# Performance work log

Measured on AMD Instinct MI355X. Metric: run time of the kernel, lower is better.

The kernel has to match this reference:

```python
import jax, jax.numpy as jnp
import numpy as np

N, F_IN, HID, PROJ, K = 10000, 256, 128, 64, 50
E, HEADS = 320000, 8


def _p(key, shape, scale=0.05):
    return jax.random.normal(key, shape, dtype=jnp.float32) * scale


def setup_inputs() -> dict:
    key = jax.random.key(0)
    ks = jax.random.split(key, 20)
    x = jax.random.normal(ks[0], (N, F_IN), dtype=jnp.float32)
    edge_index = jax.random.randint(ks[1], (2, E), 0, N, dtype=jnp.int64)
    return {
        "x": x,
        "edge_index": edge_index,
        "lin1_w": _p(ks[2], (HID, F_IN)), "lin1_b": _p(ks[3], (HID,)),
        "gat1_w": _p(ks[4], (HEADS * HID, F_IN)),
        "gat1_att_src": _p(ks[5], (HEADS, HID)), "gat1_att_dst": _p(ks[6], (HEADS, HID)),
        "gat1_b": _p(ks[7], (HEADS * HID,)),
        "gat2_w": _p(ks[8], (HID, HEADS * HID)),
        "gat2_att_src": _p(ks[9], (1, HID)), "gat2_att_dst": _p(ks[10], (1, HID)),
        "gat2_b": _p(ks[11], (HID,)),
        "proj_w": _p(ks[12], (PROJ, 2 * HID)), "proj_b": _p(ks[13], (PROJ,)),
        "ln_g": jnp.ones((2 * HID,), jnp.float32), "ln_b": jnp.zeros((2 * HID,), jnp.float32),
        "lin_w": _p(ks[14], (64, 4 * HID)), "lin_b": _p(ks[15], (64,)),
    }


def gat_conv(x, src, dst, W, a_src, a_dst, b, concat):
    # PyG GATConv, add_self_loops=False, eval mode (no attention dropout).
    H, C = a_src.shape
    n = x.shape[0]
    h = (x @ W.T).reshape(n, H, C)                      # [N,H,C]
    al_src = jnp.einsum('nhc,hc->nh', h, a_src)          # [N,H]
    al_dst = jnp.einsum('nhc,hc->nh', h, a_dst)
    e = jax.nn.leaky_relu(al_src[src] + al_dst[dst], 0.2)  # [E,H]
    emax = jax.ops.segment_max(e, dst, num_segments=n)
    ex = jnp.exp(e - emax[dst])
    denom = jax.ops.segment_sum(ex, dst, num_segments=n) + 1e-16
    alpha = ex / denom[dst]                              # [E,H]
    out = jax.ops.segment_sum(h[src] * alpha[:, :, None], dst, num_segments=n)  # [N,H,C]
    if concat:
        return out.reshape(n, H * C) + b
    return out.mean(axis=1) + b


def knn_mean(g_score, final, k):
    # dense pairwise sq-distance + top-k (replaces CPU KDTree loop), gather-mean
    sq = jnp.sum(g_score * g_score, axis=1)
    neg_d2 = 2.0 * (g_score @ g_score.T) - sq[:, None] - sq[None, :]
    idx = jax.lax.top_k(jax.lax.stop_gradient(neg_d2), k)[1]  # [N,k]
    return jnp.mean(final[idx], axis=1)                        # [N,2h]


def reference(x, edge_index, lin1_w, lin1_b, gat1_w, gat1_att_src, gat1_att_dst,
              gat1_b, gat2_w, gat2_att_src, gat2_att_dst, gat2_b, proj_w, proj_b,
              ln_g, ln_b, lin_w, lin_b):
    src, dst = edge_index[0], edge_index[1]
    x1 = jax.nn.relu(x @ lin1_w.T + lin1_b)                              # MLP branch
    xg = jax.nn.relu(gat_conv(x, src, dst, gat1_w, gat1_att_src, gat1_att_dst, gat1_b, True))
    x2 = gat_conv(xg, src, dst, gat2_w, gat2_att_src, gat2_att_dst, gat2_b, False)
    final = jnp.concatenate([x1, x2], axis=1)                            # [N,2h]
    g_score = final @ proj_w.T + proj_b                                  # [N,proj]
    sim = knn_mean(g_score, final, K)                                    # [N,2h]
    mu = sim.mean(axis=-1, keepdims=True)
    var = sim.var(axis=-1, keepdims=True)
    sim = (sim - mu) * jax.lax.rsqrt(var + 1e-5) * ln_g + ln_b           # LayerNorm
    out = jnp.concatenate([final, sim], axis=1) @ lin_w.T + lin_b        # [N,64]
    return out
```

## Files before the change

kernel.cpp:

```cpp
#include <hip/hip_runtime.h>

#define FIN 256
#define KNN 50
#define JB  2000
#define CAP 128

static __device__ __forceinline__ float lrelu02(float v){ return v > 0.f ? v : 0.2f*v; }
static __device__ __forceinline__ unsigned fkey(float v){
  unsigned u = __float_as_uint(v);
  return (u & 0x80000000u) ? ~u : (u | 0x80000000u);
}

__global__ __launch_bounds__(256) void k_zero_int(int* p, int n){
  int i = blockIdx.x*256 + threadIdx.x; if (i<n) p[i]=0;
}
__global__ __launch_bounds__(256) void k_count_deg(const int* __restrict__ dstv, int* deg, int E){
  int i = blockIdx.x*256 + threadIdx.x; if (i<E) atomicAdd(&deg[dstv[i]], 1);
}
__global__ __launch_bounds__(256) void k_scan(const int* __restrict__ deg, int* offs, int* cursor, int n){
  __shared__ int buf[256]; __shared__ int carry;
  int t = threadIdx.x;
  if (t==0) carry = 0;
  __syncthreads();
  for (int base=0; base<n; base+=256){
    int v = (base+t<n)? deg[base+t] : 0;
    buf[t]=v; __syncthreads();
    for (int off=1; off<256; off<<=1){
      int add = (t>=off)? buf[t-off] : 0;
      __syncthreads();
      buf[t]+=add; __syncthreads();
    }
    int excl = buf[t]-v+carry;
    if (base+t<n){ offs[base+t]=excl; cursor[base+t]=excl; }
    __syncthreads();
    if (t==0) carry += buf[255];
    __syncthreads();
  }
}
__global__ __launch_bounds__(256) void k_fill_csr(const int* __restrict__ dstv, int* cursor, int* csr, int E){
  int i = blockIdx.x*256 + threadIdx.x;
  if (i<E){ int p=atomicAdd(&cursor[dstv[i]],1); csr[p]=i; }
}
__global__ __launch_bounds__(64) void k_sort_csr_wave(int* csr, const int* __restrict__ offs, const int* __restrict__ deg, int n){
  int node = blockIdx.x; if (node>=n) return;
  int t = threadIdx.x;
  int st = offs[node], d = deg[node];
  __shared__ int buf[256];
  if (d > 256){
    if (t==0){
      for (int a=1;a<d;++a){ int v=csr[st+a]; int b=a-1;
        while (b>=0 && csr[st+b]>v){ csr[st+b+1]=csr[st+b]; --b; }
        csr[st+b+1]=v; }
    }
    return;
  }
  for (int q=t;q<d;q+=64) buf[q]=csr[st+q];
  __syncthreads();
  for (int it=0; it<d; ++it){
    int ph = it & 1;
    for (int pidx=t; 2*pidx+ph+1 < d; pidx+=64){
      int a = 2*pidx+ph;
      int va=buf[a], vb=buf[a+1];
      if (va > vb){ buf[a]=vb; buf[a+1]=va; }
    }
    __syncthreads();
  }
  for (int q=t;q<d;q+=64) csr[st+q]=buf[q];
}

__global__ __launch_bounds__(256) void k_fold(
  const float* __restrict__ W, const float* __restrict__ as8, const float* __restrict__ ad8,
  float* __restrict__ Wf)
{
  int o = blockIdx.x;
  int t = threadIdx.x;
  int h = o & 7;
  const float* av = (o<8) ? (as8 + h*128) : (ad8 + h*128);
  const float* wp = W + (size_t)h*128*256 + t;
  float acc = 0.f;
  #pragma unroll 4
  for (int c=0;c<128;++c) acc += av[c] * wp[(size_t)c*256];
  Wf[o*256+t] = acc;
}

__global__ __launch_bounds__(256) void gemm_bt(
    const float* __restrict__ A, int lda,
    const float* __restrict__ W, int ldw,
    const float* __restrict__ bias,
    float* __restrict__ C, int ldc, int coff,
    int M, int Kdim, int O, int relu,
    int az, int wz, int cz, int bz)
{
  A += (size_t)blockIdx.z * az;
  W += (size_t)blockIdx.z * wz;
  if (bias) bias += (size_t)blockIdx.z * bz;
  coff += blockIdx.z * cz;
  __shared__ float As[32][68];
  __shared__ float Ws[32][68];
  int t  = threadIdx.x;
  int n0 = blockIdx.y * 64;
  int o0 = blockIdx.x * 64;
  int tx = t & 15, ty = t >> 4;
  float acc[4][4] = {};
  int kgrp = t & 7;
  int row  = t >> 3;
  for (int k0 = 0; k0 < Kdim; k0 += 32) {
    #pragma unroll
    for (int p = 0; p < 2; ++p) {
      int r = row + 32*p;
      int n = n0 + r;
      float4 v = make_float4(0.f,0.f,0.f,0.f);
      if (n < M) v = *(const float4*)(A + (size_t)n*lda + k0 + 4*kgrp);
      As[4*kgrp+0][r] = v.x; As[4*kgrp+1][r] = v.y;
      As[4*kgrp+2][r] = v.z; As[4*kgrp+3][r] = v.w;
      int o = o0 + r;
      float4 w = make_float4(0.f,0.f,0.f,0.f);
      if (o < O) w = *(const float4*)(W + (size_t)o*ldw + k0 + 4*kgrp);
      Ws[4*kgrp+0][r] = w.x; Ws[4*kgrp+1][r] = w.y;
      Ws[4*kgrp+2][r] = w.z; Ws[4*kgrp+3][r] = w.w;
    }
    __syncthreads();
    #pragma unroll 8
    for (int kk = 0; kk < 32; ++kk) {
      float4 a = *(const float4*)&As[kk][ty*4];
      float4 w = *(const float4*)&Ws[kk][tx*4];
      float av[4] = {a.x,a.y,a.z,a.w};
      float wv[4] = {w.x,w.y,w.z,w.w};
      #pragma unroll
      for (int i=0;i<4;++i)
        #pragma unroll
        for (int j=0;j<4;++j) acc[i][j] += av[i]*wv[j];
    }
    __syncthreads();
  }
  #pragma unroll
  for (int i=0;i<4;++i) {
    int n = n0 + ty*4 + i;
    if (n >= M) continue;
    #pragma unroll
    for (int j=0;j<4;++j) {
      int o = o0 + tx*4 + j;
      if (o >= O) continue;
      float v = acc[i][j] + (bias ? bias[o] : 0.f);
      if (relu) v = fmaxf(v, 0.f);
      C[(size_t)n*ldc + coff + o] = v;
    }
  }
}

__global__ __launch_bounds__(256) void gemm128(
    const float* __restrict__ A, int lda,
    const float* __restrict__ W, int ldw,
    const float* __restrict__ bias,
    float* __restrict__ C, int ldc, int coff,
    int M, int Kdim, int relu,
    int az, int wz, int cz, int bz)
{
  A += (size_t)blockIdx.z * az;
  W += (size_t)blockIdx.z * wz;
  const float* bp = bias + (size_t)blockIdx.z * bz;
  int ccol = coff + blockIdx.z * cz;
  __shared__ float As[32][132];
  __shared__ float Ws[32][132];
  int t = threadIdx.x;
  int n0 = blockIdx.y * 128;
  int kg = t & 7, rb = t >> 3;
  int tx = t & 15, ty = t >> 4;
  float acc[2][2][4][4] = {};
  for (int k0 = 0; k0 < Kdim; k0 += 32) {
    __syncthreads();
    #pragma unroll
    for (int p = 0; p < 4; ++p) {
      int r = rb + 32*p;
      int n = n0 + r;
      float4 v = make_float4(0.f,0.f,0.f,0.f);
      if (n < M) v = *(const float4*)(A + (size_t)n*lda + k0 + 4*kg);
      As[4*kg+0][r]=v.x; As[4*kg+1][r]=v.y; As[4*kg+2][r]=v.z; As[4*kg+3][r]=v.w;
      float4 w = *(const float4*)(W + (size_t)r*ldw + k0 + 4*kg);
      Ws[4*kg+0][r]=w.x; Ws[4*kg+1][r]=w.y; Ws[4*kg+2][r]=w.z; Ws[4*kg+3][r]=w.w;
    }
    __syncthreads();
    #pragma unroll 8
    for (int kk = 0; kk < 32; ++kk) {
      float4 A0 = *(const float4*)&As[kk][ty*4];
      float4 A1 = *(const float4*)&As[kk][64+ty*4];
      float4 B0 = *(const float4*)&Ws[kk][tx*4];
      float4 B1 = *(const float4*)&Ws[kk][64+tx*4];
      float av[2][4] = {{A0.x,A0.y,A0.z,A0.w},{A1.x,A1.y,A1.z,A1.w}};
      float bv[2][4] = {{B0.x,B0.y,B0.z,B0.w},{B1.x,B1.y,B1.z,B1.w}};
      #pragma unroll
      for (int pi=0;pi<2;++pi)
        #pragma unroll
        for (int pj=0;pj<2;++pj)
          #pragma unroll
          for (int i=0;i<4;++i)
            #pragma unroll
            for (int j=0;j<4;++j)
              acc[pi][pj][i][j] += av[pi][i]*bv[pj][j];
    }
  }
  #pragma unroll
  for (int pi=0;pi<2;++pi)
    #pragma unroll
    for (int i=0;i<4;++i) {
      int n = n0 + pi*64 + ty*4 + i;
      if (n >= M) continue;
      #pragma unroll
      for (int pj=0;pj<2;++pj)
        #pragma unroll
        for (int j=0;j<4;++j) {
          int o = pj*64 + tx*4 + j;
          float v = acc[pi][pj][i][j] + bp[o];
          if (relu) v = fmaxf(v, 0.f);
          C[(size_t)n*ldc + ccol + o] = v;
        }
    }
}

__global__ __launch_bounds__(256) void att_logits(
    const float* __restrict__ hbuf, const float* __restrict__ asrc,
    const float* __restrict__ adst, float* __restrict__ als, float* __restrict__ ald,
    int H, int M)
{
  int gidx = blockIdx.x*256 + threadIdx.x;
  if (gidx >= M*H) return;
  int n = gidx / H, h = gidx % H;
  const float* hp = hbuf + (size_t)n*H*128 + (size_t)h*128;
  const float* as = asrc + h*128;
  const float* ad = adst + h*128;
  float s1=0.f, s2=0.f;
  for (int c=0;c<128;++c){ float v=hp[c]; s1 += v*as[c]; s2 += v*ad[c]; }
  als[gidx]=s1; ald[gidx]=s2;
}

template<int NH>
__global__ __launch_bounds__(256) void gat1_agg_x(
    const float* __restrict__ x, const float* __restrict__ al1,
    const int* __restrict__ csr, const int* __restrict__ offs, const int* __restrict__ deg,
    const int* __restrict__ srcv,
    float* __restrict__ agg, int h0, int M)
{
  const int n = blockIdx.x, t = threadIdx.x;
  const int d = deg[n], st = offs[n];
  const int lane = t & 63, w = t >> 6;
  __shared__ float sh_ald[NH];
  __shared__ float wpart[4*NH];
  __shared__ float emax_s[NH], den_s[NH];
  __shared__ int   s_lds[128];
  __shared__ float alpha_lds[128*NH];
  if (t < NH) sh_ald[t] = al1[(size_t)n*16 + 8 + h0 + t];
  __syncthreads();
  float lm[NH];
  #pragma unroll
  for (int h=0;h<NH;++h) lm[h] = -__builtin_inff();
  for (int q=t; q<d; q+=256) {
    int s = srcv[csr[st+q]];
    float av[NH];
    float4 a0 = *(const float4*)(al1 + (size_t)s*16 + h0);
    av[0]=a0.x; av[1]=a0.y; av[2]=a0.z; av[3]=a0.w;
    if constexpr (NH==8){
      float4 a1 = *(const float4*)(al1 + (size_t)s*16 + h0 + 4);
      av[4]=a1.x; av[5]=a1.y; av[6]=a1.z; av[7]=a1.w;
    }
    #pragma unroll
    for (int h=0;h<NH;++h) lm[h] = fmaxf(lm[h], lrelu02(av[h] + sh_ald[h]));
  }
  #pragma unroll
  for (int h=0;h<NH;++h){
    float v = lm[h];
    for (int off=32;off>0;off>>=1) v = fmaxf(v, __shfl_down(v, off, 64));
    if (lane==0) wpart[w*NH+h] = v;
  }
  __syncthreads();
  if (t < NH)
    emax_s[t] = fmaxf(fmaxf(wpart[t], wpart[NH+t]), fmaxf(wpart[2*NH+t], wpart[3*NH+t]));
  __syncthreads();
  float ls[NH];
  #pragma unroll
  for (int h=0;h<NH;++h) ls[h]=0.f;
  for (int q=t; q<d; q+=256) {
    int s = srcv[csr[st+q]];
    float av[NH];
    float4 a0 = *(const float4*)(al1 + (size_t)s*16 + h0);
    av[0]=a0.x; av[1]=a0.y; av[2]=a0.z; av[3]=a0.w;
    if constexpr (NH==8){
      float4 a1 = *(const float4*)(al1 + (size_t)s*16 + h0 + 4);
      av[4]=a1.x; av[5]=a1.y; av[6]=a1.z; av[7]=a1.w;
    }
    #pragma unroll
    for (int h=0;h<NH;++h) ls[h] += expf(lrelu02(av[h] + sh_ald[h]) - emax_s[h]);
  }
  #pragma unroll
  for (int h=0;h<NH;++h){
    float v = ls[h];
    for (int off=32;off>0;off>>=1) v += __shfl_down(v, off, 64);
    if (lane==0) wpart[w*NH+h] = v;
  }
  __syncthreads();
  if (t < NH)
    den_s[t] = wpart[t] + wpart[NH+t] + wpart[2*NH+t] + wpart[3*NH+t] + 1e-16f;
  float acc[NH];
  #pragma unroll
  for (int h=0;h<NH;++h) acc[h]=0.f;
  for (int c0=0; c0<d; c0+=128) {
    int cl = min(128, d-c0);
    __syncthreads();
    for (int q=t; q<cl; q+=256) s_lds[q] = srcv[csr[st+c0+q]];
    __syncthreads();
    for (int idx=t; idx<cl*NH; idx+=256) {
      int q = idx / NH, h = idx % NH;
      float als = al1[(size_t)s_lds[q]*16 + h0 + h];
      float v = lrelu02(als + sh_ald[h]);
      alpha_lds[q*NH+h] = expf(v - emax_s[h]) / den_s[h];
    }
    __syncthreads();
    for (int q=0; q<cl; ++q) {
      float xv = x[(size_t)s_lds[q]*FIN + t];
      #pragma unroll
      for (int h=0;h<NH;++h) acc[h] += alpha_lds[q*NH+h] * xv;
    }
  }
  #pragma unroll
  for (int h=0;h<NH;++h) agg[(size_t)n*(NH*256) + h*256 + t] = acc[h];
}

__global__ __launch_bounds__(256) void gat2_agg_wave(
  const float* __restrict__ h2, const float* __restrict__ als, const float* __restrict__ ald,
  const int* __restrict__ csr, const int* __restrict__ offs, const int* __restrict__ deg,
  const int* __restrict__ srcv, const float* __restrict__ bias,
  float* __restrict__ cat, int M)
{
  int wid = blockIdx.x*4 + (threadIdx.x>>6);
  int lane = threadIdx.x & 63;
  if (wid >= M) return;
  int d = deg[wid], st = offs[wid];
  float aldn = ald[wid];
  float lm = -__builtin_inff();
  for (int q=lane;q<d;q+=64){ int s=srcv[csr[st+q]]; lm = fmaxf(lm, lrelu02(als[s]+aldn)); }
  #pragma unroll
  for (int m=1;m<64;m<<=1) lm = fmaxf(lm, __shfl_xor(lm, m, 64));
  float ls = 0.f;
  for (int q=lane;q<d;q+=64){ int s=srcv[csr[st+q]]; ls += expf(lrelu02(als[s]+aldn)-lm); }
  #pragma unroll
  for (int m=1;m<64;m<<=1) ls += __shfl_xor(ls, m, 64);
  float den = ls + 1e-16f;
  float a0=0.f, a1=0.f;
  for (int q=0;q<d;++q){
    int s = srcv[csr[st+q]];
    float alpha = expf(lrelu02(als[s]+aldn)-lm)/den;
    float2 hv = *(const float2*)(h2 + (size_t)s*128 + lane*2);
    a0 += alpha*hv.x; a1 += alpha*hv.y;
  }
  a0 += bias[lane*2]; a1 += bias[lane*2+1];
  *(float2*)(cat + (size_t)wid*512 + 128 + lane*2) = make_float2(a0,a1);
}

__global__ __launch_bounds__(256) void k_sq(const float* __restrict__ g, float* sq, int n){
  int i = blockIdx.x*256+threadIdx.x;
  if (i<n){ const float* p=g+(size_t)i*64; float s=0.f; for(int c=0;c<64;++c) s+=p[c]*p[c]; sq[i]=s; }
}
__global__ __launch_bounds__(256) void k_init_topk(unsigned int* tk, int* ti, int n){
  int i = blockIdx.x*256+threadIdx.x;
  if (i<n){ tk[i]=0u; ti[i]=0x7fffffff; }
}

template<int MODE>
__global__ __launch_bounds__(256) void gram128v4(
    const float* __restrict__ G, const float* __restrict__ sqv,
    const unsigned* __restrict__ kth,
    float* __restrict__ slab, int* __restrict__ cnt,
    unsigned* __restrict__ ck, int* __restrict__ ci,
    int j0, int M)
{
  __shared__ float4 GiS[32*16];
  __shared__ float4 GjS[32*32];
  float* Gif = (float*)GiS;
  float* Gjf = (float*)GjS;
  int t = threadIdx.x;
  int i0  = blockIdx.y * 64;
  int jt0 = blockIdx.x * 128;
  int tx = t & 15, ty = t >> 4;
  int kg = t & 7, rw = t >> 3;
  float acc[2][4][4] = {};
  #pragma unroll
  for (int h=0; h<2; ++h) {
    if (h) __syncthreads();
    #pragma unroll
    for (int rr=0; rr<2; ++rr) {
      int r = rw + 32*rr;
      int slotA = (r>>2) ^ kg;
      int gi = i0 + r;
      float4 v = (gi<M) ? *(const float4*)(G + (size_t)gi*64 + h*32 + 4*kg) : make_float4(0,0,0,0);
      Gif[((4*kg+0)*16 + slotA)*4 + (r&3)] = v.x;
      Gif[((4*kg+1)*16 + slotA)*4 + (r&3)] = v.y;
      Gif[((4*kg+2)*16 + slotA)*4 + (r&3)] = v.z;
      Gif[((4*kg+3)*16 + slotA)*4 + (r&3)] = v.w;
    }
    #pragma unroll
    for (int rr=0; rr<4; ++rr) {
      int r = rw + 32*rr;
      int slotB = (r>>2) ^ kg;
      int gj = j0 + jt0 + r;
      float4 w = (gj<M) ? *(const float4*)(G + (size_t)gj*64 + h*32 + 4*kg) : make_float4(0,0,0,0);
      Gjf[((4*kg+0)*32 + slotB)*4 + (r&3)] = w.x;
      Gjf[((4*kg+1)*32 + slotB)*4 + (r&3)] = w.y;
      Gjf[((4*kg+2)*32 + slotB)*4 + (r&3)] = w.z;
      Gjf[((4*kg+3)*32 + slotB)*4 + (r&3)] = w.w;
    }
    __syncthreads();
    #pragma unroll 8
    for (int k=0; k<32; ++k) {
      int kc3 = (k>>2)&7;
      int sa = ty ^ kc3;
      int sb = tx ^ kc3;
      float4 A0 = GiS[k*16 + sa];
      float4 B0 = GjS[k*32 + sb];
      float4 B1 = GjS[k*32 + 16 + sb];
      float av[4] = {A0.x,A0.y,A0.z,A0.w};
      float bv[2][4] = {{B0.x,B0.y,B0.z,B0.w},{B1.x,B1.y,B1.z,B1.w}};
      #pragma unroll
      for (int pj=0;pj<2;++pj)
        #pragma unroll
        for (int i=0;i<4;++i)
          #pragma unroll
          for (int j=0;j<4;++j)
            acc[pj][i][j] += av[i]*bv[pj][j];
    }
  }
  #pragma unroll
  for (int i=0;i<4;++i){
    int ii = i0 + ty*4 + i;
    if (ii >= M) continue;
    float sqi = sqv[ii];
    #pragma unroll
    for (int pj=0;pj<2;++pj){
      int jl0 = jt0 + pj*64 + tx*4;
      if (jl0 >= JB) continue;
      float4 v4;
      v4.x = 2.f*acc[pj][i][0] - sqi - sqv[j0+jl0+0];
      v4.y = 2.f*acc[pj][i][1] - sqi - sqv[j0+jl0+1];
      v4.z = 2.f*acc[pj][i][2] - sqi - sqv[j0+jl0+2];
      v4.w = 2.f*acc[pj][i][3] - sqi - sqv[j0+jl0+3];
      if (MODE == 0) {
        *(float4*)(slab + (size_t)ii*JB + jl0) = v4;
      } else {
        unsigned kt = kth[ii];
        float vv[4] = {v4.x, v4.y, v4.z, v4.w};
        #pragma unroll
        for (int j=0;j<4;++j){
          unsigned key = fkey(vv[j]);
          if (key > kt){
            int pos = atomicAdd(&cnt[ii], 1);
            if (pos < CAP){ ck[(size_t)ii*CAP+pos] = key; ci[(size_t)ii*CAP+pos] = j0+jl0+j; }
          }
        }
      }
    }
  }
}

__global__ __launch_bounds__(256) void topk_radix(
    const float* __restrict__ slab, int j0, int jcount,
    unsigned* __restrict__ tkk, int* __restrict__ tki, unsigned* __restrict__ kth, int M)
{
  __shared__ unsigned keys[JB + KNN];
  __shared__ int hist[256];
  __shared__ int red2[256];
  __shared__ int oldidx[KNN];
  __shared__ int outidx[KNN];
  __shared__ unsigned outkey[KNN];
  __shared__ int b_star, cnt2;
  int i = blockIdx.x, t = threadIdx.x;
  for (int p=t; p<jcount; p+=256) keys[p] = fkey(slab[(size_t)i*JB + p]);
  for (int p=jcount+t; p<JB; p+=256) keys[p] = 0u;
  if (t < KNN){ keys[JB+t] = tkk[(size_t)i*KNN+t]; oldidx[t] = tki[(size_t)i*KNN+t]; }
  if (t == 0) cnt2 = 0;
  __syncthreads();
  const int total = JB + KNN;
  unsigned prefix = 0, pmask = 0;
  int need = KNN;
  #pragma unroll
  for (int pass=0; pass<4; ++pass) {
    int shift = 24 - 8*pass;
    hist[t] = 0; __syncthreads();
    for (int p=t; p<total; p+=256) {
      unsigned k = keys[p];
      if ((k & pmask) == prefix) atomicAdd(&hist[(k>>shift)&255], 1);
    }
    __syncthreads();
    for (int off=1; off<256; off<<=1) {
      int v = (t+off<256) ? hist[t+off] : 0;
      __syncthreads();
      hist[t] += v;
      __syncthreads();
    }
    if (hist[t] >= need && (t==255 || hist[t+1] < need)) b_star = t;
    __syncthreads();
    int b = b_star;
    need -= (b < 255) ? hist[b+1] : 0;
    prefix |= ((unsigned)b) << shift;
    pmask  |= 0xFFu << shift;
    __syncthreads();
  }
  for (int p=t; p<total; p+=256) {
    unsigned k = keys[p];
    if (k > prefix) {
      int pos = atomicAdd(&cnt2, 1);
      outidx[pos] = (p < JB) ? (j0 + p) : oldidx[p-JB];
      outkey[pos] = k;
    }
  }
  __syncthreads();
  int base = cnt2;
  int last = -1;
  for (int it=0; it<need; ++it) {
    int best = 0x7fffffff;
    for (int p=t; p<total; p+=256) {
      if (keys[p] == prefix) {
        int idx = (p < JB) ? (j0 + p) : oldidx[p-JB];
        if (idx > last && idx < best) best = idx;
      }
    }
    red2[t] = best; __syncthreads();
    for (int s=128;s>0;s>>=1){ if (t<s) red2[t] = min(red2[t], red2[t+s]); __syncthreads(); }
    if (t==0) { outidx[base+it] = red2[0]; outkey[base+it] = prefix; }
    last = red2[0];
    __syncthreads();
  }
  if (t < KNN){ tkk[(size_t)i*KNN+t] = outkey[t]; tki[(size_t)i*KNN+t] = outidx[t]; }
  if (t == 0) kth[i] = prefix;
}

__global__ __launch_bounds__(256) void topk_fast(
    const float* __restrict__ G, const float* __restrict__ sqv,
    int j0, int jcount,
    const unsigned* __restrict__ ck, const int* __restrict__ ci, const int* __restrict__ cnt,
    unsigned* __restrict__ tkk, int* __restrict__ tki, unsigned* __restrict__ kth, int M)
{
  int i = blockIdx.x, t = threadIdx.x;
  int c = cnt[i];
  if (c <= CAP) {
    __shared__ unsigned skey[256];
    __shared__ int sidx[256];
    unsigned k = 0u; int id = 0x7fffffff;
    if (t < KNN){ k = tkk[(size_t)i*KNN+t]; id = tki[(size_t)i*KNN+t]; }
    else if (t-KNN < c){ k = ck[(size_t)i*CAP + (t-KNN)]; id = ci[(size_t)i*CAP + (t-KNN)]; }
    skey[t] = k; sidx[t] = id;
    for (int size=2; size<=256; size<<=1){
      for (int stride=size>>1; stride>0; stride>>=1){
        __syncthreads();
        int p = t ^ stride;
        if (p > t){
          unsigned k1=skey[t], k2=skey[p]; int i1=sidx[t], i2=sidx[p];
          bool b21 = (k2>k1) || (k2==k1 && i2<i1);
          bool b12 = (k1>k2) || (k1==k2 && i1<i2);
          bool desc = ((t & size) == 0);
          if (desc ? b21 : b12){
            skey[t]=k2; skey[p]=k1; sidx[t]=i2; sidx[p]=i1;
          }
        }
      }
    }
    __syncthreads();
    if (t < KNN){ tkk[(size_t)i*KNN+t] = skey[t]; tki[(size_t)i*KNN+t] = sidx[t]; }
    if (t == 0) kth[i] = skey[KNN-1];
  } else {
    __shared__ float gvec[64];
    __shared__ unsigned keys[JB + KNN];
    __shared__ int hist[256];
    __shared__ int red2[256];
    __shared__ int oldidx[KNN];
    __shared__ int outidx[KNN];
    __shared__ unsigned outkey[KNN];
    __shared__ int b_star, cnt2;
    if (t < 64) gvec[t] = G[(size_t)i*64 + t];
    if (t == 0) cnt2 = 0;
    __syncthreads();
    float sqi = sqv[i];
    for (int p=t; p<jcount; p+=256){
      const float4* gj4 = (const float4*)(G + (size_t)(j0+p)*64);
      float acc = 0.f;
      #pragma unroll 4
      for (int q=0;q<16;++q){
        float4 w = gj4[q];
        acc += gvec[4*q+0]*w.x;
        acc += gvec[4*q+1]*w.y;
        acc += gvec[4*q+2]*w.z;
        acc += gvec[4*q+3]*w.w;
      }
      keys[p] = fkey(2.f*acc - sqi - sqv[j0+p]);
    }
    for (int p=jcount+t; p<JB; p+=256) keys[p] = 0u;
    if (t < KNN){ keys[JB+t] = tkk[(size_t)i*KNN+t]; oldidx[t] = tki[(size_t)i*KNN+t]; }
    __syncthreads();
    const int total = JB + KNN;
    unsigned prefix = 0, pmask = 0;
    int need = KNN;
    #pragma unroll
    for (int pass=0; pass<4; ++pass) {
      int shift = 24 - 8*pass;
      hist[t] = 0; __syncthreads();
      for (int p=t; p<total; p+=256) {
        unsigned k = keys[p];
        if ((k & pmask) == prefix) atomicAdd(&hist[(k>>shift)&255], 1);
      }
      __syncthreads();
      for (int off=1; off<256; off<<=1) {
        int v = (t+off<256) ? hist[t+off] : 0;
        __syncthreads();
        hist[t] += v;
        __syncthreads();
      }
      if (hist[t] >= need && (t==255 || hist[t+1] < need)) b_star = t;
      __syncthreads();
      int b = b_star;
      need -= (b < 255) ? hist[b+1] : 0;
      prefix |= ((unsigned)b) << shift;
      pmask  |= 0xFFu << shift;
      __syncthreads();
    }
    for (int p=t; p<total; p+=256) {
      unsigned k = keys[p];
      if (k > prefix) {
        int pos = atomicAdd(&cnt2, 1);
        outidx[pos] = (p < JB) ? (j0 + p) : oldidx[p-JB];
        outkey[pos] = k;
      }
    }
    __syncthreads();
    int base = cnt2;
    int last = -1;
    for (int it=0; it<need; ++it) {
      int best = 0x7fffffff;
      for (int p=t; p<total; p+=256) {
        if (keys[p] == prefix) {
          int idx = (p < JB) ? (j0 + p) : oldidx[p-JB];
          if (idx > last && idx < best) best = idx;
        }
      }
      red2[t] = best; __syncthreads();
      for (int s=128;s>0;s>>=1){ if (t<s) red2[t] = min(red2[t], red2[t+s]); __syncthreads(); }
      if (t==0) { outidx[base+it] = red2[0]; outkey[base+it] = prefix; }
      last = red2[0];
      __syncthreads();
    }
    if (t < KNN){ tkk[(size_t)i*KNN+t] = outkey[t]; tki[(size_t)i*KNN+t] = outidx[t]; }
    if (t == 0) kth[i] = prefix;
  }
}

__global__ __launch_bounds__(256) void knn_mean_ln(
    float* __restrict__ cat, const int* __restrict__ topi,
    const float* __restrict__ g, const float* __restrict__ b, int M)
{
  int i = blockIdx.x; int t = threadIdx.x;
  __shared__ int idx[KNN];
  __shared__ float red[256];
  if (t<KNN) idx[t]=topi[(size_t)i*KNN+t];
  __syncthreads();
  float acc=0.f;
  for (int r=0;r<KNN;++r) acc += cat[(size_t)idx[r]*512 + t];
  float xval = acc * (1.f/KNN);
  red[t]=xval; __syncthreads();
  for (int s=128;s>0;s>>=1){ if(t<s) red[t]+=red[t+s]; __syncthreads(); }
  float mu = red[0]*(1.f/256.f); __syncthreads();
  float d = xval-mu;
  red[t]=d*d; __syncthreads();
  for (int s=128;s>0;s>>=1){ if(t<s) red[t]+=red[t+s]; __syncthreads(); }
  float var = red[0]*(1.f/256.f);
  float y = d * rsqrtf(var+1e-5f) * g[t] + b[t];
  cat[(size_t)i*512 + 256 + t] = y;
}

extern "C" void kernel_launch(void* const* d_in, const int* in_sizes, int n_in,
                              void* d_out, int out_size, void* d_ws, size_t ws_size,
                              hipStream_t stream)
{
  const float* x      = (const float*)d_in[0];
  const int*   ei     = (const int*)  d_in[1];
  const float* lin1_w = (const float*)d_in[2];
  const float* lin1_b = (const float*)d_in[3];
  const float* gat1_w = (const float*)d_in[4];
  const float* g1_as  = (const float*)d_in[5];
  const float* g1_ad  = (const float*)d_in[6];
  const float* gat1_b = (const float*)d_in[7];
  const float* gat2_w = (const float*)d_in[8];
  const float* g2_as  = (const float*)d_in[9];
  const float* g2_ad  = (const float*)d_in[10];
  const float* gat2_b = (const float*)d_in[11];
  const float* proj_w = (const float*)d_in[12];
  const float* proj_b = (const float*)d_in[13];
  const float* ln_g   = (const float*)d_in[14];
  const float* ln_b   = (const float*)d_in[15];
  const float* lin_w  = (const float*)d_in[16];
  const float* lin_b  = (const float*)d_in[17];
  float* outp = (float*)d_out;

  const int N = in_sizes[0]/FIN;
  const int E = in_sizes[1]/2;
  const int* srcv = ei;
  const int* dstv = ei + E;

  size_t needFull = sizeof(float)*((size_t)N*(2048+1024+512+16+128+1+1+64+1+KNN+KNN+1+1+1+1+1+2*CAP) + E + 4096);
  bool full = ws_size >= needFull;
  size_t aggF = full ? (size_t)N*2048 : (size_t)N*1024;

  float* ws = (float*)d_ws;
  size_t f = 0;
  float* agg  = ws + f; f += aggF;
  float* xg   = ws + f; f += (size_t)N*1024;
  float* slab = agg;
  float* cat  = ws + f; f += (size_t)N*512;
  float* al1  = ws + f; f += (size_t)N*16;
  float* h2   = ws + f; f += (size_t)N*128;
  float* al2s = ws + f; f += (size_t)N;
  float* al2d = ws + f; f += (size_t)N;
  float* gsc  = ws + f; f += (size_t)N*64;
  float* sqv  = ws + f; f += (size_t)N;
  unsigned* tkk = (unsigned*)(ws + f); f += (size_t)N*KNN;
  int* tki    = (int*)(ws + f); f += (size_t)N*KNN;
  int* deg    = (int*)(ws + f); f += (size_t)N;
  int* offs   = (int*)(ws + f); f += (size_t)N;
  int* cursor = (int*)(ws + f); f += (size_t)N;
  unsigned* kth = (unsigned*)(ws + f); f += (size_t)N;
  int* ccnt   = (int*)(ws + f); f += (size_t)N;
  unsigned* ck = (unsigned*)(ws + f); f += (size_t)N*CAP;
  int* ci     = (int*)(ws + f); f += (size_t)N*CAP;
  int* csr    = (int*)(ws + f); f += (size_t)E;
  float* Wf   = ws + f; f += 4096;
  (void)n_in; (void)out_size;

  dim3 b256(256);
  int gy = (N+63)/64;
  int gy128 = (N+127)/128;
  int gy64 = (N+63)/64;

  k_zero_int<<<(N+255)/256, b256, 0, stream>>>(deg, N);
  k_count_deg<<<(E+255)/256, b256, 0, stream>>>(dstv, deg, E);
  k_scan<<<1, b256, 0, stream>>>(deg, offs, cursor, N);
  k_fill_csr<<<(E+255)/256, b256, 0, stream>>>(dstv, cursor, csr, E);
  k_sort_csr_wave<<<N, dim3(64), 0, stream>>>(csr, offs, deg, N);

  k_fold<<<16, b256, 0, stream>>>(gat1_w, g1_as, g1_ad, Wf);
  gemm_bt<<<dim3(1,gy,1), b256, 0, stream>>>(x,FIN, Wf,FIN, nullptr, al1,16,0, N,FIN,16, 0, 0,0,0,0);

  gemm_bt<<<dim3(2,gy,1), b256, 0, stream>>>(x,FIN, lin1_w,FIN, lin1_b, cat,512,0, N,FIN,128, 1, 0,0,0,0);

  if (full) {
    gat1_agg_x<8><<<N, b256, 0, stream>>>(x, al1, csr, offs, deg, srcv, agg, 0, N);
    gemm128<<<dim3(1,gy128,8), b256, 0, stream>>>(agg,2048, gat1_w,FIN, gat1_b, xg,1024,0,
                                                  N,FIN, 1, 256, 128*256, 128, 128);
  } else {
    for (int h0=0; h0<8; h0+=4) {
      gat1_agg_x<4><<<N, b256, 0, stream>>>(x, al1, csr, offs, deg, srcv, agg, h0, N);
      gemm128<<<dim3(1,gy128,4), b256, 0, stream>>>(agg,1024, gat1_w + (size_t)h0*128*256,FIN,
                                                    gat1_b + h0*128, xg,1024, h0*128,
                                                    N,FIN, 1, 256, 128*256, 128, 128);
    }
  }

  gemm_bt<<<dim3(2,gy,1), b256, 0, stream>>>(xg,1024, gat2_w,1024, nullptr, h2,128,0, N,1024,128, 0, 0,0,0,0);
  att_logits<<<(N+255)/256, b256, 0, stream>>>(h2, g2_as, g2_ad, al2s, al2d, 1, N);
  gat2_agg_wave<<<(N+3)/4, b256, 0, stream>>>(h2, al2s, al2d, csr, offs, deg, srcv, gat2_b, cat, N);

  gemm_bt<<<dim3(1,gy,1), b256, 0, stream>>>(cat,512, proj_w,256, proj_b, gsc,64,0, N,256,64, 0, 0,0,0,0);
  k_sq<<<(N+255)/256, b256, 0, stream>>>(gsc, sqv, N);
  k_init_topk<<<(N*KNN+255)/256, b256, 0, stream>>>(tkk, tki, N*KNN);
  for (int j0=0; j0<N; j0+=JB){
    int jc = (N - j0 < JB) ? (N - j0) : JB;
    if (j0 == 0) {
      gram128v4<0><<<dim3((JB+127)/128, gy64), b256, 0, stream>>>(gsc, sqv, kth, slab, ccnt, ck, ci, j0, N);
      topk_radix<<<N, b256, 0, stream>>>(slab, j0, jc, tkk, tki, kth, N);
    } else {
      k_zero_int<<<(N+255)/256, b256, 0, stream>>>(ccnt, N);
      gram128v4<1><<<dim3((JB+127)/128, gy64), b256, 0, stream>>>(gsc, sqv, kth, slab, ccnt, ck, ci, j0, N);
      topk_fast<<<N, b256, 0, stream>>>(gsc, sqv, j0, jc, ck, ci, ccnt, tkk, tki, kth, N);
    }
  }
  knn_mean_ln<<<N, b256, 0, stream>>>(cat, tki, ln_g, ln_b, N);
  gemm_bt<<<dim3(1,gy,1), b256, 0, stream>>>(cat,512, lin_w,512, lin_b, outp,64,0, N,512,64, 0, 0,0,0,0);
}
```

Before: 1.257 ms.

## Use geometrically growing kNN column chunks with a small first radix pass

Replaces the fixed 2000-column kNN chunking with five chunks of growing size (512, 1024, 2048, 3208, 3208). The first chunk, which needs the full slab write and radix select, is now small. Later chunks use the threshold-filtered candidate path, where the kth-best key tightens quickly, so fewer candidates should pass. The radix histogram is split into per-wave copies to reduce shared-atomic contention, and the padding of unused key slots is removed. The trade-offs are more kernel launches, a larger shared key buffer in the fallback path (lower occupancy), and a larger candidate CAP, so a bigger chunk may overflow the candidate buffer more often.

```diff
diff --git a/kernel.cpp b/kernel.cpp
--- a/kernel.cpp
+++ b/kernel.cpp
@@ -2,8 +2,9 @@
 
 #define FIN 256
 #define KNN 50
-#define JB  2000
-#define CAP 128
+#define CAP 192
+#define J1  512
+#define MAXJC 3208
 
 static __device__ __forceinline__ float lrelu02(float v){ return v > 0.f ? v : 0.2f*v; }
 static __device__ __forceinline__ unsigned fkey(float v){
@@ -370,7 +371,7 @@
     const unsigned* __restrict__ kth,
     float* __restrict__ slab, int* __restrict__ cnt,
     unsigned* __restrict__ ck, int* __restrict__ ci,
-    int j0, int M)
+    int j0, int jcount, int M)
 {
   __shared__ float4 GiS[32*16];
   __shared__ float4 GjS[32*32];
@@ -435,14 +436,14 @@
     #pragma unroll
     for (int pj=0;pj<2;++pj){
       int jl0 = jt0 + pj*64 + tx*4;
-      if (jl0 >= JB) continue;
+      if (jl0 >= jcount) continue;
       float4 v4;
       v4.x = 2.f*acc[pj][i][0] - sqi - sqv[j0+jl0+0];
       v4.y = 2.f*acc[pj][i][1] - sqi - sqv[j0+jl0+1];
       v4.z = 2.f*acc[pj][i][2] - sqi - sqv[j0+jl0+2];
       v4.w = 2.f*acc[pj][i][3] - sqi - sqv[j0+jl0+3];
       if (MODE == 0) {
-        *(float4*)(slab + (size_t)ii*JB + jl0) = v4;
+        *(float4*)(slab + (size_t)ii*J1 + jl0) = v4;
       } else {
         unsigned kt = kth[ii];
         float vv[4] = {v4.x, v4.y, v4.z, v4.w};
@@ -463,41 +464,43 @@
     const float* __restrict__ slab, int j0, int jcount,
     unsigned* __restrict__ tkk, int* __restrict__ tki, unsigned* __restrict__ kth, int M)
 {
-  __shared__ unsigned keys[JB + KNN];
-  __shared__ int hist[256];
+  __shared__ unsigned keys[J1 + KNN];
+  __shared__ int hist[4*256];
   __shared__ int red2[256];
   __shared__ int oldidx[KNN];
   __shared__ int outidx[KNN];
   __shared__ unsigned outkey[KNN];
   __shared__ int b_star, cnt2;
-  int i = blockIdx.x, t = threadIdx.x;
-  for (int p=t; p<jcount; p+=256) keys[p] = fkey(slab[(size_t)i*JB + p]);
-  for (int p=jcount+t; p<JB; p+=256) keys[p] = 0u;
-  if (t < KNN){ keys[JB+t] = tkk[(size_t)i*KNN+t]; oldidx[t] = tki[(size_t)i*KNN+t]; }
+  int i = blockIdx.x, t = threadIdx.x, w = t >> 6;
+  for (int p=t; p<jcount; p+=256) keys[p] = fkey(slab[(size_t)i*J1 + p]);
+  if (t < KNN){ keys[jcount+t] = tkk[(size_t)i*KNN+t]; oldidx[t] = tki[(size_t)i*KNN+t]; }
   if (t == 0) cnt2 = 0;
   __syncthreads();
-  const int total = JB + KNN;
+  const int total = jcount + KNN;
   unsigned prefix = 0, pmask = 0;
   int need = KNN;
   #pragma unroll
   for (int pass=0; pass<4; ++pass) {
     int shift = 24 - 8*pass;
-    hist[t] = 0; __syncthreads();
+    hist[t]=0; hist[256+t]=0; hist[512+t]=0; hist[768+t]=0;
+    __syncthreads();
     for (int p=t; p<total; p+=256) {
       unsigned k = keys[p];
-      if ((k & pmask) == prefix) atomicAdd(&hist[(k>>shift)&255], 1);
-    }
+      if ((k & pmask) == prefix) atomicAdd(&hist[(w<<8) + ((k>>shift)&255)], 1);
+    }
+    __syncthreads();
+    red2[t] = hist[t] + hist[256+t] + hist[512+t] + hist[768+t];
     __syncthreads();
     for (int off=1; off<256; off<<=1) {
-      int v = (t+off<256) ? hist[t+off] : 0;
+      int v = (t+off<256) ? red2[t+off] : 0;
       __syncthreads();
-      hist[t] += v;
+      red2[t] += v;
       __syncthreads();
     }
-    if (hist[t] >= need && (t==255 || hist[t+1] < need)) b_star = t;
+    if (red2[t] >= need && (t==255 || red2[t+1] < need)) b_star = t;
     __syncthreads();
     int b = b_star;
-    need -= (b < 255) ? hist[b+1] : 0;
+    need -= (b < 255) ? red2[b+1] : 0;
     prefix |= ((unsigned)b) << shift;
     pmask  |= 0xFFu << shift;
     __syncthreads();
@@ -506,7 +509,7 @@
     unsigned k = keys[p];
     if (k > prefix) {
       int pos = atomicAdd(&cnt2, 1);
-      outidx[pos] = (p < JB) ? (j0 + p) : oldidx[p-JB];
+      outidx[pos] = (p < jcount) ? (j0 + p) : oldidx[p-jcount];
       outkey[pos] = k;
     }
   }
@@ -517,7 +520,7 @@
     int best = 0x7fffffff;
     for (int p=t; p<total; p+=256) {
       if (keys[p] == prefix) {
-        int idx = (p < JB) ? (j0 + p) : oldidx[p-JB];
+        int idx = (p < jcount) ? (j0 + p) : oldidx[p-jcount];
         if (idx > last && idx < best) best = idx;
       }
     }
@@ -566,7 +569,7 @@
     if (t == 0) kth[i] = skey[KNN-1];
   } else {
     __shared__ float gvec[64];
-    __shared__ unsigned keys[JB + KNN];
+    __shared__ unsigned keys[MAXJC + KNN];
     __shared__ int hist[256];
     __shared__ int red2[256];
     __shared__ int oldidx[KNN];
@@ -590,10 +593,9 @@
       }
       keys[p] = fkey(2.f*acc - sqi - sqv[j0+p]);
     }
-    for (int p=jcount+t; p<JB; p+=256) keys[p] = 0u;
-    if (t < KNN){ keys[JB+t] = tkk[(size_t)i*KNN+t]; oldidx[t] = tki[(size_t)i*KNN+t]; }
-    __syncthreads();
-    const int total = JB + KNN;
+    if (t < KNN){ keys[jcount+t] = tkk[(size_t)i*KNN+t]; oldidx[t] = tki[(size_t)i*KNN+t]; }
+    __syncthreads();
+    const int total = jcount + KNN;
     unsigned prefix = 0, pmask = 0;
     int need = KNN;
     #pragma unroll
@@ -623,7 +625,7 @@
       unsigned k = keys[p];
       if (k > prefix) {
         int pos = atomicAdd(&cnt2, 1);
-        outidx[pos] = (p < JB) ? (j0 + p) : oldidx[p-JB];
+        outidx[pos] = (p < jcount) ? (j0 + p) : oldidx[p-jcount];
         outkey[pos] = k;
       }
     }
@@ -634,7 +636,7 @@
       int best = 0x7fffffff;
       for (int p=t; p<total; p+=256) {
         if (keys[p] == prefix) {
-          int idx = (p < JB) ? (j0 + p) : oldidx[p-JB];
+          int idx = (p < jcount) ? (j0 + p) : oldidx[p-jcount];
           if (idx > last && idx < best) best = idx;
         }
       }
@@ -766,14 +768,20 @@
   gemm_bt<<<dim3(1,gy,1), b256, 0, stream>>>(cat,512, proj_w,256, proj_b, gsc,64,0, N,256,64, 0, 0,0,0,0);
   k_sq<<<(N+255)/256, b256, 0, stream>>>(gsc, sqv, N);
   k_init_topk<<<(N*KNN+255)/256, b256, 0, stream>>>(tkk, tki, N*KNN);
-  for (int j0=0; j0<N; j0+=JB){
-    int jc = (N - j0 < JB) ? (N - j0) : JB;
-    if (j0 == 0) {
-      gram128v4<0><<<dim3((JB+127)/128, gy64), b256, 0, stream>>>(gsc, sqv, kth, slab, ccnt, ck, ci, j0, N);
+  k_zero_int<<<(N+255)/256, b256, 0, stream>>>((int*)kth, N);
+
+  const int sj0[5] = {0, 512, 1536, 3584, 6792};
+  const int sjc[5] = {512, 1024, 2048, 3208, 3208};
+  for (int s = 0; s < 5; ++s){
+    int j0 = sj0[s], jc = sjc[s];
+    if (jc > N - j0) jc = N - j0;
+    if (jc <= 0) break;
+    if (s == 0) {
+      gram128v4<0><<<dim3((jc+127)/128, gy64), b256, 0, stream>>>(gsc, sqv, kth, slab, ccnt, ck, ci, j0, jc, N);
       topk_radix<<<N, b256, 0, stream>>>(slab, j0, jc, tkk, tki, kth, N);
     } else {
       k_zero_int<<<(N+255)/256, b256, 0, stream>>>(ccnt, N);
-      gram128v4<1><<<dim3((JB+127)/128, gy64), b256, 0, stream>>>(gsc, sqv, kth, slab, ccnt, ck, ci, j0, N);
+      gram128v4<1><<<dim3((jc+127)/128, gy64), b256, 0, stream>>>(gsc, sqv, kth, slab, ccnt, ck, ci, j0, jc, N);
       topk_fast<<<N, b256, 0, stream>>>(gsc, sqv, j0, jc, ck, ci, ccnt, tkk, tki, kth, N);
     }
   }
```

After: 1.264 ms. No clear change (+0.5%).
